# Performance work log

Measured on AMD Instinct MI355X. Metric: run time of the kernel, lower is better.

## Reference

```python
import jax, jax.numpy as jnp
import numpy as np

HEADS = 20
SHIFT = 0.6931471805599453  # style_alignment_score_shift = log(2)
KEY_SCALE = 1.0             # style_alignment_score_scale
EPS = 1e-5


def expand_first(feat, scale=1.0):
    # feat: [B, H, S, D]; broadcast style features (batch items 0 and B//2)
    b = feat.shape[0]
    fs = jnp.stack([feat[0], feat[b // 2]])[:, None]           # [2,1,H,S,D]
    fs = jnp.broadcast_to(fs, (2, b // 2) + feat.shape[1:])    # [2,B/2,H,S,D]
    if scale != 1:
        fs = jnp.concatenate([fs[:, :1], scale * fs[:, 1:]], axis=1)
    return fs.reshape(feat.shape)


def concat_first(feat, scale=1.0):
    # concatenate style features along the sequence axis (-2)
    return jnp.concatenate([feat, expand_first(feat, scale=scale)], axis=-2)


def adain(feat):
    # stats over sequence axis (-2); torch .var() is unbiased (ddof=1)
    mean = feat.mean(axis=-2, keepdims=True)
    std = jnp.sqrt(feat.var(axis=-2, keepdims=True, ddof=1) + EPS)
    sm = expand_first(mean)
    ss = expand_first(std)
    return (feat - mean) / std * ss + sm


def setup_inputs() -> dict:
    key = jax.random.key(0)
    ks = jax.random.split(key, 6)
    B, S, C = 4, 1024, 1280
    sc = 1.0 / np.sqrt(C)
    return {
        "hidden_states": jax.random.normal(ks[0], (B, S, C), jnp.float32),
        "Wq": jax.random.normal(ks[1], (C, C), jnp.float32) * sc,
        "Wk": jax.random.normal(ks[2], (C, C), jnp.float32) * sc,
        "Wv": jax.random.normal(ks[3], (C, C), jnp.float32) * sc,
        "Wo": jax.random.normal(ks[4], (C, C), jnp.float32) * sc,
        "bo": jnp.zeros((C,), jnp.float32),
    }


def reference(hidden_states, Wq, Wk, Wv, Wo, bo):
    B, S, C = hidden_states.shape
    H = HEADS
    hd = C // H
    scale = hd ** -0.5

    def to_heads(t):  # [B,S,C] -> [B,H,S,hd]
        return t.reshape(B, S, H, hd).transpose(0, 2, 1, 3)

    q = to_heads(hidden_states @ Wq.T)
    k = to_heads(hidden_states @ Wk.T)
    v = to_heads(hidden_states @ Wv.T)

    q = adain(q)              # adain_queries
    k = adain(k)              # adain_keys
    # adain_values = False

    k = concat_first(k, scale=KEY_SCALE)   # [B,H,2S,hd]
    v = concat_first(v)                    # [B,H,2S,hd]

    # shifted scaled dot-product attention (shift added to shared-key block)
    logits = jnp.einsum('bhqd,bhkd->bhqk', q, k) * scale  # [B,H,S,2S]
    bias = jnp.where(jnp.arange(k.shape[-2]) >= S, jnp.float32(SHIFT), jnp.float32(0.0))
    probs = jax.nn.softmax(logits + bias, axis=-1)
    out = jnp.einsum('bhqk,bhkd->bhqd', probs, v)         # [B,H,S,hd]

    out = out.transpose(0, 2, 1, 3).reshape(B, S, C)
    out = out @ Wo.T + bo
    return out
```

## Files before the change

kernel.cpp:

```cpp
#include <hip/hip_runtime.h>
#include <math.h>


typedef __bf16 bf16x8 __attribute__((ext_vector_type(8)));
typedef __bf16 bf16x2_t __attribute__((ext_vector_type(2)));
typedef float f32x4 __attribute__((ext_vector_type(4)));
typedef unsigned short u16x8 __attribute__((ext_vector_type(8)));

#define BDIM 256

__device__ inline unsigned short f2bf(float f) {
  return __builtin_bit_cast(unsigned short, (__bf16)f);
}
__device__ inline unsigned int pack_bf2(float lo, float hi) {
  bf16x2_t v;
  v[0] = (__bf16)lo;
  v[1] = (__bf16)hi;
  return __builtin_bit_cast(unsigned int, v);
}
__device__ inline float bf2f(unsigned short h) {
  return __uint_as_float(((unsigned int)h) << 16);
}

__device__ inline void gl_lds16(const unsigned short* g, unsigned short* l) {
  __builtin_amdgcn_global_load_lds(
      (const __attribute__((address_space(1))) unsigned int*)g,
      (__attribute__((address_space(3))) unsigned int*)l, 16, 0, 0);
}

__global__ __launch_bounds__(BDIM) void k_convert_all(
    const float* __restrict__ X, const float* __restrict__ Wq,
    const float* __restrict__ Wk, const float* __restrict__ Wv,
    const float* __restrict__ Wo, unsigned short* __restrict__ Xbf,
    unsigned short* __restrict__ Wcat, unsigned short* __restrict__ Wobf) {
  const int idx = blockIdx.x * BDIM + threadIdx.x;
  const float* src;
  unsigned short* dst;
  int off;
  if (idx < 1310720) {
    src = X; dst = Xbf; off = idx;
  } else {
    const int r = idx - 1310720;
    const int which = r / 409600;
    off = r - which * 409600;
    src = (which == 0) ? Wq : (which == 1) ? Wk : (which == 2) ? Wv : Wo;
    dst = (which < 3) ? Wcat + (size_t)which * 1638400 : Wobf;
  }
  const float4 v = ((const float4*)src)[off];
  ushort4 o;
  o.x = f2bf(v.x); o.y = f2bf(v.y); o.z = f2bf(v.z); o.w = f2bf(v.w);
  ((ushort4*)dst)[off] = o;
}

__global__ __launch_bounds__(512, 1) void k_gemm_bf16(
    const unsigned short* __restrict__ A, const unsigned short* __restrict__ B,
    unsigned short* __restrict__ Cbf, int M, int N, int K) {
  __shared__ unsigned short lds[2][2][16384];

  const int bid = blockIdx.x;
  const int swz = (bid & 7) * 30 + (bid >> 3);
  const int mt = swz & 15, nt = swz >> 4;
  const int mBase = mt * 256, nBase = nt * 256;

  const int t = threadIdx.x;
  const int w = t >> 6, lane = t & 63, quad = lane >> 4, l16 = lane & 15;
  const int wrow = w & 1, wcol = w >> 1;
  const int glg = (lane & 7) ^ ((lane >> 3) & 7);
  const int NTILES = K >> 6;

  f32x4 acc[8][4];
#pragma unroll
  for (int i = 0; i < 8; ++i)
#pragma unroll
    for (int j = 0; j < 4; ++j) acc[i][j] = (f32x4){0.f, 0.f, 0.f, 0.f};

  auto stage = [&](int s, int kt) {
#pragma unroll
    for (int j = 0; j < 4; ++j) {
      const int row = j * 64 + w * 8 + (lane >> 3);
      gl_lds16(A + (size_t)(mBase + row) * K + kt * 64 + glg * 8,
               &lds[s][0][(j * 512 + w * 64 + lane) * 8]);
    }
#pragma unroll
    for (int j = 0; j < 4; ++j) {
      const int row = j * 64 + w * 8 + (lane >> 3);
      gl_lds16(B + (size_t)(nBase + row) * K + kt * 64 + glg * 8,
               &lds[s][1][(j * 512 + w * 64 + lane) * 8]);
    }
  };

  stage(0, 0);
  stage(1, 1);
  asm volatile("s_waitcnt vmcnt(8)" ::: "memory");
  __builtin_amdgcn_s_barrier();

  const int arow0 = (wrow * 128 + l16) * 64;
  const int brow0 = (wcol * 64 + l16) * 64;
  const int g0 = ((quad) ^ (l16 & 7)) * 8;
  const int g1 = ((4 + quad) ^ (l16 & 7)) * 8;

  for (int kt = 0; kt < NTILES; ++kt) {
    const int s = kt & 1;
    if (kt >= 1 && kt + 1 < NTILES) stage(s ^ 1, kt + 1);
    const unsigned short* As = &lds[s][0][0];
    const unsigned short* Bs = &lds[s][1][0];
#pragma unroll
    for (int ph = 0; ph < 4; ++ph) {
      const int mh = ph >> 1, nh = ph & 1;
      bf16x8 af[4][2], bq[2][2];
#pragma unroll
      for (int mi = 0; mi < 4; ++mi) {
        const int ro = arow0 + (mh * 4 + mi) * 1024;
        af[mi][0] = *(const bf16x8*)(As + ro + g0);
        af[mi][1] = *(const bf16x8*)(As + ro + g1);
      }
#pragma unroll
      for (int ni = 0; ni < 2; ++ni) {
        const int ro = brow0 + (nh * 2 + ni) * 1024;
        bq[ni][0] = *(const bf16x8*)(Bs + ro + g0);
        bq[ni][1] = *(const bf16x8*)(Bs + ro + g1);
      }
      __builtin_amdgcn_s_setprio(1);
#pragma unroll
      for (int kk = 0; kk < 2; ++kk)
#pragma unroll
        for (int mi = 0; mi < 4; ++mi)
#pragma unroll
          for (int ni = 0; ni < 2; ++ni)
            acc[mh * 4 + mi][nh * 2 + ni] =
                __builtin_amdgcn_mfma_f32_16x16x32_bf16(
                    af[mi][kk], bq[ni][kk], acc[mh * 4 + mi][nh * 2 + ni], 0,
                    0, 0);
      __builtin_amdgcn_s_setprio(0);
      if (ph < 3) __builtin_amdgcn_s_barrier();
    }
    asm volatile("s_waitcnt vmcnt(0)" ::: "memory");
    __builtin_amdgcn_s_barrier();
  }

#pragma unroll
  for (int mi = 0; mi < 8; ++mi)
#pragma unroll
    for (int r = 0; r < 4; ++r) {
      const int row = mBase + wrow * 128 + mi * 16 + quad * 4 + r;
#pragma unroll
      for (int ni = 0; ni < 4; ++ni)
        Cbf[(size_t)row * N + nBase + wcol * 64 + ni * 16 + l16] =
            f2bf(acc[mi][ni][r]);
    }
}

__global__ __launch_bounds__(BDIM) void k_gemm_64x128(
    const unsigned short* __restrict__ A, const unsigned short* __restrict__ B,
    float* __restrict__ Cf, const float* __restrict__ bias, int M, int N,
    int K) {
  __shared__ unsigned short As[2][64 * 32];
  __shared__ unsigned short Bs[2][128 * 32];
  const int t = threadIdx.x;
  const int w = t >> 6, lane = t & 63, quad = lane >> 4, l16 = lane & 15;
  const int wm = (w >> 1) << 5, wn = (w & 1) << 6;
  const int mBase = blockIdx.x * 64, nBase = blockIdx.y * 128;

  f32x4 acc[2][4];
#pragma unroll
  for (int i = 0; i < 2; i++)
#pragma unroll
    for (int j = 0; j < 4; j++) acc[i][j] = (f32x4){0.f, 0.f, 0.f, 0.f};

  const int r0 = t >> 2;
  const int kk0 = (t & 3) * 8;

  for (int k0 = 0; k0 < K; k0 += 64) {
    const unsigned short* Ab = A + (size_t)(mBase + r0) * K + k0 + kk0;
    const unsigned short* Bb = B + (size_t)(nBase + r0) * K + k0 + kk0;
    gl_lds16(Ab, As[0] + t * 8);
    gl_lds16(Ab + 32, As[1] + t * 8);
    gl_lds16(Bb, Bs[0] + t * 8);
    gl_lds16(Bb + (size_t)64 * K, Bs[0] + (t + 256) * 8);
    gl_lds16(Bb + 32, Bs[1] + t * 8);
    gl_lds16(Bb + (size_t)64 * K + 32, Bs[1] + (t + 256) * 8);
    __syncthreads();
    bf16x8 af[2][2], bfr[2][4];
#pragma unroll
    for (int hh = 0; hh < 2; hh++) {
#pragma unroll
      for (int i = 0; i < 2; i++)
        af[hh][i] = *(const bf16x8*)(As[hh] + (wm + i * 16 + l16) * 32 + quad * 8);
#pragma unroll
      for (int i = 0; i < 4; i++)
        bfr[hh][i] = *(const bf16x8*)(Bs[hh] + (wn + i * 16 + l16) * 32 + quad * 8);
    }
#pragma unroll
    for (int hh = 0; hh < 2; hh++)
#pragma unroll
      for (int mi = 0; mi < 2; mi++)
#pragma unroll
        for (int ni = 0; ni < 4; ni++)
          acc[mi][ni] = __builtin_amdgcn_mfma_f32_16x16x32_bf16(
              af[hh][mi], bfr[hh][ni], acc[mi][ni], 0, 0, 0);
    __syncthreads();
  }

#pragma unroll
  for (int mi = 0; mi < 2; mi++)
#pragma unroll
    for (int r = 0; r < 4; r++) {
      const int row = mBase + wm + mi * 16 + quad * 4 + r;
#pragma unroll
      for (int ni = 0; ni < 4; ni++) {
        const int col = nBase + wn + ni * 16 + l16;
        Cf[(size_t)row * N + col] = acc[mi][ni][r] + bias[col];
      }
    }
}

__global__ __launch_bounds__(320) void k_stats1(
    const unsigned short* __restrict__ QKV, float* __restrict__ psum,
    float* __restrict__ psq) {
  const int z = blockIdx.y, which = z >> 2, b = z & 3;
  const int c = threadIdx.x * 4;
  const size_t base =
      (size_t)(b * 1024 + blockIdx.x * 32) * 3840 + which * 1280 + c;
  float4 s = {0.f, 0.f, 0.f, 0.f}, s2 = {0.f, 0.f, 0.f, 0.f};
#pragma unroll 8
  for (int i = 0; i < 32; ++i) {
    const ushort4 xv = *(const ushort4*)(QKV + base + (size_t)i * 3840);
    const float x0 = bf2f(xv.x), x1 = bf2f(xv.y), x2 = bf2f(xv.z),
                x3 = bf2f(xv.w);
    s.x += x0; s.y += x1; s.z += x2; s.w += x3;
    s2.x = fmaf(x0, x0, s2.x); s2.y = fmaf(x1, x1, s2.y);
    s2.z = fmaf(x2, x2, s2.z); s2.w = fmaf(x3, x3, s2.w);
  }
  const size_t o = ((size_t)z * 32 + blockIdx.x) * 1280 + c;
  *(float4*)(psum + o) = s;
  *(float4*)(psq + o) = s2;
}

__global__ __launch_bounds__(BDIM) void k_stats2(
    const float* __restrict__ psum, const float* __restrict__ psq,
    float* __restrict__ stats) {
  const int z = blockIdx.y, which = z >> 2, b = z & 3;
  const int c = blockIdx.x * 256 + threadIdx.x;
  float s = 0.f, s2 = 0.f;
#pragma unroll
  for (int j = 0; j < 32; ++j) {
    s += psum[((size_t)z * 32 + j) * 1280 + c];
    s2 += psq[((size_t)z * 32 + j) * 1280 + c];
  }
  const float mean = s * (1.0f / 1024.0f);
  const float var = (s2 - 1024.0f * mean * mean) * (1.0f / 1023.0f);
  stats[((which * 2 + 0) * 4 + b) * 1280 + c] = mean;
  stats[((which * 2 + 1) * 4 + b) * 1280 + c] = sqrtf(var + 1e-5f);
}

__global__ __launch_bounds__(BDIM) void k_adain_vt(
    const unsigned short* __restrict__ QKV, const float* __restrict__ stats,
    unsigned short* __restrict__ qn, unsigned short* __restrict__ kn,
    unsigned short* __restrict__ vt) {
  __shared__ unsigned short tile[64][65];
  const int bx = blockIdx.x;
  if (bx < 10240) {
    const int which = bx / 5120;
    const int rem = bx - which * 5120;
    const int b = rem / 1280;
    const int xb = rem - b * 1280;
    const int idx = xb * BDIM + threadIdx.x;
    const int s = idx / 320;
    const int c = (idx - s * 320) * 4;
    const int sb = (b < 2) ? 0 : 2;
    const ushort4 xv = *(const ushort4*)(QKV + ((size_t)(b * 1024 + s)) * 3840 +
                                         which * 1280 + c);
    const float4 mean =
        *(const float4*)(stats + ((which * 2 + 0) * 4 + b) * 1280 + c);
    const float4 stdv =
        *(const float4*)(stats + ((which * 2 + 1) * 4 + b) * 1280 + c);
    const float4 meanS =
        *(const float4*)(stats + ((which * 2 + 0) * 4 + sb) * 1280 + c);
    const float4 stdS =
        *(const float4*)(stats + ((which * 2 + 1) * 4 + sb) * 1280 + c);
    ushort4 o;
    o.x = f2bf((bf2f(xv.x) - mean.x) / stdv.x * stdS.x + meanS.x);
    o.y = f2bf((bf2f(xv.y) - mean.y) / stdv.y * stdS.y + meanS.y);
    o.z = f2bf((bf2f(xv.z) - mean.z) / stdv.z * stdS.z + meanS.z);
    o.w = f2bf((bf2f(xv.w) - mean.w) / stdv.w * stdS.w + meanS.w);
    unsigned short* dst = (which == 0) ? qn : kn;
    *(ushort4*)(dst + ((size_t)(b * 1024 + s)) * 1280 + c) = o;
  } else {
    const int tb = bx - 10240;
    const int b = tb / 320;
    const int r2 = tb - b * 320;
    const int c0 = (r2 / 16) * 64;
    const int s0 = (r2 & 15) * 64;
    const int t = threadIdx.x;
    const int r = t >> 2, seg = (t & 3) * 16;
    const size_t goff = ((size_t)(b * 1024 + s0 + r)) * 3840 + 2560 + c0 + seg;
    const u16x8 va = *(const u16x8*)(QKV + goff);
    const u16x8 vb = *(const u16x8*)(QKV + goff + 8);
#pragma unroll
    for (int j = 0; j < 8; j++) {
      tile[r][seg + j] = va[j];
      tile[r][seg + 8 + j] = vb[j];
    }
    __syncthreads();
    u16x8 o0, o1;
#pragma unroll
    for (int j = 0; j < 8; j++) {
      o0[j] = tile[seg + j][r];
      o1[j] = tile[seg + 8 + j][r];
    }
    const size_t ooff = ((size_t)(b * 1280 + c0 + r)) * 1024 + s0 + seg;
    *(u16x8*)(vt + ooff) = o0;
    *(u16x8*)(vt + ooff + 8) = o1;
  }
}

__global__ __launch_bounds__(BDIM, 4) void k_attn(
    const unsigned short* __restrict__ qn, const unsigned short* __restrict__ kn,
    const unsigned short* __restrict__ vt, unsigned short* __restrict__ Opart,
    float* __restrict__ Lpart) {
  const int S = 1024, C = 1280;
  const int L = blockIdx.x + 8 * (blockIdx.y + 20 * blockIdx.z);
  const int qt = (L >> 3) & 7;
  const int hz = (L & 7) + ((L >> 6) << 3);
  const int h = hz % 20;
  const int zs = hz / 20;
  int b, chunk;
  if (zs < 2)      { b = 0; chunk = zs; }
  else if (zs < 6) { b = 1; chunk = zs - 2; }
  else if (zs < 8) { b = 2; chunk = zs - 6; }
  else             { b = 3; chunk = zs - 8; }
  const int ktBeg = chunk * 8;
  const int t = threadIdx.x, w = t >> 6, lane = t & 63;
  const int quad = lane >> 4, l16 = lane & 15;
  const int bstyle = (b < 2) ? 0 : 2;
  const int qrow = qt * 128 + w * 32;

  __shared__ unsigned short Ks[2][2][64 * 32];
  __shared__ unsigned short Vs[2][64 * 32];
  __shared__ unsigned short Plds[4][32][64];

  bf16x8 aq[2][2];
#pragma unroll
  for (int g = 0; g < 2; ++g) {
    const size_t qoff =
        ((size_t)(b * S + qrow + g * 16 + l16)) * C + h * 64 + quad * 8;
    aq[g][0] = *(const bf16x8*)(qn + qoff);
    aq[g][1] = *(const bf16x8*)(qn + qoff + 32);
  }

  bf16x8 ones;
#pragma unroll
  for (int i = 0; i < 8; ++i) ones[i] = (__bf16)1.0f;

  f32x4 o[2][4], lsum[2];
#pragma unroll
  for (int g = 0; g < 2; ++g) {
    lsum[g] = (f32x4){0.f, 0.f, 0.f, 0.f};
#pragma unroll
    for (int i = 0; i < 4; i++) o[g][i] = (f32x4){0.f, 0.f, 0.f, 0.f};
  }

  const int krow = t >> 2;
  const int kseg = (t & 3) * 8;
  const int sw = l16 & 14;

  auto stageK = [&](int buf, int kt) {
    const int bs = (kt < 16) ? b : bstyle;
    const int sk = (kt & 15) * 64;
    const unsigned short* kg =
        kn + (size_t)(bs * S + sk + krow) * C + h * 64 + kseg;
    gl_lds16(kg, Ks[buf][0] + t * 8);
    gl_lds16(kg + 32, Ks[buf][1] + t * 8);
  };
  auto stageV = [&](int kt) {
    const int bs = (kt < 16) ? b : bstyle;
    const int sk = (kt & 15) * 64;
    const unsigned short* vg =
        vt + (size_t)(bs * C + h * 64 + krow) * S + sk + kseg;
    gl_lds16(vg, Vs[0] + t * 8);
    gl_lds16(vg + 32, Vs[1] + t * 8);
  };

  stageK(0, ktBeg);

  const float SCALE2 = 0.125f * 1.44269504088896341f;

  for (int i = 0; i < 8; ++i) {
    const int kt = ktBeg + i;
    const int buf = i & 1;
    __syncthreads();
    stageV(kt);
    if (i + 1 < 8) stageK(buf ^ 1, kt + 1);

    const float bias2 = (kt >= 16) ? 1.0f : 0.0f;

    f32x4 z2[2][4];
#pragma unroll
    for (int nt = 0; nt < 4; ++nt) {
      const bf16x8 bk0 =
          *(const bf16x8*)(Ks[buf][0] + (nt * 16 + l16) * 32 + quad * 8);
      const bf16x8 bk1 =
          *(const bf16x8*)(Ks[buf][1] + (nt * 16 + l16) * 32 + quad * 8);
#pragma unroll
      for (int g = 0; g < 2; ++g) {
        f32x4 zz = (f32x4){0.f, 0.f, 0.f, 0.f};
        zz = __builtin_amdgcn_mfma_f32_16x16x32_bf16(bk0, aq[g][0], zz, 0, 0, 0);
        zz = __builtin_amdgcn_mfma_f32_16x16x32_bf16(bk1, aq[g][1], zz, 0, 0, 0);
        z2[g][nt] = zz;
      }
    }

#pragma unroll
    for (int g = 0; g < 2; ++g) {
#pragma unroll
      for (int nt = 0; nt < 4; ++nt) {
        const float e0 = exp2f(fmaf(z2[g][nt][0], SCALE2, bias2));
        const float e1 = exp2f(fmaf(z2[g][nt][1], SCALE2, bias2));
        const float e2 = exp2f(fmaf(z2[g][nt][2], SCALE2, bias2));
        const float e3 = exp2f(fmaf(z2[g][nt][3], SCALE2, bias2));
        uint2 pk;
        pk.x = pack_bf2(e0, e1);
        pk.y = pack_bf2(e2, e3);
        const int phys = (nt * 4 + quad) ^ sw;
        *(uint2*)(&Plds[w][g * 16 + l16][phys * 4]) = pk;
      }
    }

    __syncthreads();

#pragma unroll
    for (int g = 0; g < 2; ++g) {
      const int a0 = (2 * quad) ^ sw;
      const int a1 = (2 * quad + 8) ^ sw;
      const bf16x8 pa0 = *(const bf16x8*)(&Plds[w][g * 16 + l16][a0 * 4]);
      const bf16x8 pa1 = *(const bf16x8*)(&Plds[w][g * 16 + l16][a1 * 4]);
      lsum[g] = __builtin_amdgcn_mfma_f32_16x16x32_bf16(pa0, ones, lsum[g], 0, 0, 0);
      lsum[g] = __builtin_amdgcn_mfma_f32_16x16x32_bf16(pa1, ones, lsum[g], 0, 0, 0);
#pragma unroll
      for (int dt = 0; dt < 4; ++dt) {
        const bf16x8 vb0 =
            *(const bf16x8*)(Vs[0] + (dt * 16 + l16) * 32 + quad * 8);
        const bf16x8 vb1 =
            *(const bf16x8*)(Vs[1] + (dt * 16 + l16) * 32 + quad * 8);
        o[g][dt] =
            __builtin_amdgcn_mfma_f32_16x16x32_bf16(pa0, vb0, o[g][dt], 0, 0, 0);
        o[g][dt] =
            __builtin_amdgcn_mfma_f32_16x16x32_bf16(pa1, vb1, o[g][dt], 0, 0, 0);
      }
    }
  }

  if (l16 == 0) {
#pragma unroll
    for (int g = 0; g < 2; ++g)
#pragma unroll
      for (int r = 0; r < 4; ++r)
        Lpart[((size_t)zs * 20 + h) * 1024 + qrow + g * 16 + quad * 4 + r] =
            lsum[g][r];
  }

  unsigned short* Op = Opart + (size_t)zs * 1024 * 1280;
#pragma unroll
  for (int g = 0; g < 2; ++g)
#pragma unroll
    for (int dt = 0; dt < 4; ++dt)
#pragma unroll
      for (int r = 0; r < 4; ++r)
        Op[(size_t)(qrow + g * 16 + quad * 4 + r) * 1280 + h * 64 + dt * 16 +
           l16] = f2bf(o[g][dt][r]);
}

__global__ __launch_bounds__(BDIM) void k_combine(
    const unsigned short* __restrict__ Opart, const float* __restrict__ Lpart,
    unsigned short* __restrict__ attnb) {
  const int idx = blockIdx.x * BDIM + threadIdx.x;
  const int row = idx / 160;
  const int c = (idx - row * 160) * 8;
  const int b = row >> 10, q = row & 1023, h = c >> 6;
  const int zb = (b >> 1) * 6 + (b & 1) * 2;
  const int ns = 2 + (b & 1) * 2;
  float L = 0.f;
  float acc[8] = {0.f, 0.f, 0.f, 0.f, 0.f, 0.f, 0.f, 0.f};
  for (int s = 0; s < ns; ++s) {
    L += Lpart[((size_t)(zb + s) * 20 + h) * 1024 + q];
    const u16x8 v =
        *(const u16x8*)(Opart + (size_t)(zb + s) * 1310720 + (size_t)q * 1280 + c);
#pragma unroll
    for (int j = 0; j < 8; ++j) acc[j] += bf2f(v[j]);
  }
  const float rl = 1.0f / L;
  u16x8 o8;
#pragma unroll
  for (int j = 0; j < 8; ++j) o8[j] = f2bf(acc[j] * rl);
  *(u16x8*)(attnb + (size_t)row * 1280 + c) = o8;
}

extern "C" void kernel_launch(void* const* d_in, const int* in_sizes, int n_in,
                              void* d_out, int out_size, void* d_ws,
                              size_t ws_size, hipStream_t stream) {
  const float* X = (const float*)d_in[0];
  const float* Wq = (const float*)d_in[1];
  const float* Wk = (const float*)d_in[2];
  const float* Wv = (const float*)d_in[3];
  const float* Wo = (const float*)d_in[4];
  const float* bo = (const float*)d_in[5];
  float* out = (float*)d_out;

  char* ws = (char*)d_ws;
  size_t off = 0;
  auto alloc = [&](size_t bytes) {
    char* p = ws + off;
    off += (bytes + 255) & ~(size_t)255;
    return p;
  };
  unsigned short* Wcat = (unsigned short*)alloc(3840ull * 1280 * 2);
  unsigned short* Xbf = (unsigned short*)alloc(4096ull * 1280 * 2);
  unsigned short* QKV = (unsigned short*)alloc(4096ull * 3840 * 2);
  unsigned short* Wobf = (unsigned short*)alloc(1280ull * 1280 * 2);
  float* stats = (float*)alloc(2ull * 2 * 4 * 1280 * 4);
  unsigned short* qnb = (unsigned short*)alloc(4096ull * 1280 * 2);
  unsigned short* knb = (unsigned short*)alloc(4096ull * 1280 * 2);
  unsigned short* vtb = (unsigned short*)alloc(4096ull * 1280 * 2);
  unsigned short* attnb = (unsigned short*)alloc(4096ull * 1280 * 2);

  unsigned short* Opart = QKV;
  float* Lpart = (float*)Wcat;
  float* psum = (float*)attnb;
  float* psq = (float*)(attnb + 4096ull * 1280 / 2);

  k_convert_all<<<11520, BDIM, 0, stream>>>(X, Wq, Wk, Wv, Wo, Xbf, Wcat, Wobf);
  k_gemm_bf16<<<240, 512, 0, stream>>>(Xbf, Wcat, QKV, 4096, 3840, 1280);
  k_stats1<<<dim3(32, 8), 320, 0, stream>>>(QKV, psum, psq);
  k_stats2<<<dim3(5, 8), BDIM, 0, stream>>>(psum, psq, stats);
  k_adain_vt<<<11520, BDIM, 0, stream>>>(QKV, stats, qnb, knb, vtb);
  k_attn<<<dim3(8, 20, 12), BDIM, 0, stream>>>(qnb, knb, vtb, Opart, Lpart);
  k_combine<<<2560, BDIM, 0, stream>>>(Opart, Lpart, attnb);
  k_gemm_64x128<<<dim3(64, 10), BDIM, 0, stream>>>(attnb, Wobf, out, bo, 4096,
                                                   1280, 1280);
}
```

Before: 263.4 us.

## Retile output GEMM to 128x128 with prefetch pipeline and shrink attention P buffer

Replaces the 64x128 output projection GEMM with a 128x128 tile kernel. The new kernel double-buffers K tiles, prefetching the next tile while computing the current one. It also uses XOR-swizzled LDS addressing, a block-index swizzle for cache locality, and MFMA priority hints. This is meant to raise operand reuse and overlap loads with MFMA work. The attention kernel now writes and consumes the probability tile one 16-row group at a time, halving its per-warp LDS buffer so it can target five blocks per CU. The risks are that 320 large tiles may fill the GPU unevenly, and that the serialized P handling adds latency inside each wave.

```diff
diff --git a/kernel.cpp b/kernel.cpp
--- a/kernel.cpp
+++ b/kernel.cpp
@@ -150,65 +150,98 @@
     }
 }
 
-__global__ __launch_bounds__(BDIM) void k_gemm_64x128(
+__global__ __launch_bounds__(BDIM, 2) void k_gemm_out(
     const unsigned short* __restrict__ A, const unsigned short* __restrict__ B,
     float* __restrict__ Cf, const float* __restrict__ bias, int M, int N,
     int K) {
-  __shared__ unsigned short As[2][64 * 32];
-  __shared__ unsigned short Bs[2][128 * 32];
+  __shared__ unsigned short lds[2][2][8192];
+
+  const int bid = blockIdx.x;
+  const int swz = (bid & 7) * 40 + (bid >> 3);
+  const int mt = swz & 31, nt = swz >> 5;
+  const int mBase = mt * 128, nBase = nt * 128;
+
   const int t = threadIdx.x;
   const int w = t >> 6, lane = t & 63, quad = lane >> 4, l16 = lane & 15;
-  const int wm = (w >> 1) << 5, wn = (w & 1) << 6;
-  const int mBase = blockIdx.x * 64, nBase = blockIdx.y * 128;
-
-  f32x4 acc[2][4];
-#pragma unroll
-  for (int i = 0; i < 2; i++)
-#pragma unroll
-    for (int j = 0; j < 4; j++) acc[i][j] = (f32x4){0.f, 0.f, 0.f, 0.f};
-
-  const int r0 = t >> 2;
-  const int kk0 = (t & 3) * 8;
-
-  for (int k0 = 0; k0 < K; k0 += 64) {
-    const unsigned short* Ab = A + (size_t)(mBase + r0) * K + k0 + kk0;
-    const unsigned short* Bb = B + (size_t)(nBase + r0) * K + k0 + kk0;
-    gl_lds16(Ab, As[0] + t * 8);
-    gl_lds16(Ab + 32, As[1] + t * 8);
-    gl_lds16(Bb, Bs[0] + t * 8);
-    gl_lds16(Bb + (size_t)64 * K, Bs[0] + (t + 256) * 8);
-    gl_lds16(Bb + 32, Bs[1] + t * 8);
-    gl_lds16(Bb + (size_t)64 * K + 32, Bs[1] + (t + 256) * 8);
-    __syncthreads();
-    bf16x8 af[2][2], bfr[2][4];
-#pragma unroll
-    for (int hh = 0; hh < 2; hh++) {
-#pragma unroll
-      for (int i = 0; i < 2; i++)
-        af[hh][i] = *(const bf16x8*)(As[hh] + (wm + i * 16 + l16) * 32 + quad * 8);
-#pragma unroll
-      for (int i = 0; i < 4; i++)
-        bfr[hh][i] = *(const bf16x8*)(Bs[hh] + (wn + i * 16 + l16) * 32 + quad * 8);
-    }
-#pragma unroll
-    for (int hh = 0; hh < 2; hh++)
-#pragma unroll
-      for (int mi = 0; mi < 2; mi++)
-#pragma unroll
-        for (int ni = 0; ni < 4; ni++)
-          acc[mi][ni] = __builtin_amdgcn_mfma_f32_16x16x32_bf16(
-              af[hh][mi], bfr[hh][ni], acc[mi][ni], 0, 0, 0);
-    __syncthreads();
-  }
-
-#pragma unroll
-  for (int mi = 0; mi < 2; mi++)
-#pragma unroll
-    for (int r = 0; r < 4; r++) {
-      const int row = mBase + wm + mi * 16 + quad * 4 + r;
-#pragma unroll
-      for (int ni = 0; ni < 4; ni++) {
-        const int col = nBase + wn + ni * 16 + l16;
+  const int wrow = w & 1, wcol = w >> 1;
+  const int glg = (lane & 7) ^ ((lane >> 3) & 7);
+  const int NTILES = K >> 6;
+
+  f32x4 acc[4][4];
+#pragma unroll
+  for (int i = 0; i < 4; ++i)
+#pragma unroll
+    for (int j = 0; j < 4; ++j) acc[i][j] = (f32x4){0.f, 0.f, 0.f, 0.f};
+
+  auto stage = [&](int s, int kt) {
+#pragma unroll
+    for (int j = 0; j < 4; ++j) {
+      const int row = j * 32 + (t >> 3);
+      gl_lds16(A + (size_t)(mBase + row) * K + kt * 64 + glg * 8,
+               &lds[s][0][(j * 256 + t) * 8]);
+    }
+#pragma unroll
+    for (int j = 0; j < 4; ++j) {
+      const int row = j * 32 + (t >> 3);
+      gl_lds16(B + (size_t)(nBase + row) * K + kt * 64 + glg * 8,
+               &lds[s][1][(j * 256 + t) * 8]);
+    }
+  };
+
+  stage(0, 0);
+  stage(1, 1);
+  asm volatile("s_waitcnt vmcnt(8)" ::: "memory");
+  __builtin_amdgcn_s_barrier();
+
+  const int arow0 = (wrow * 64 + l16) * 64;
+  const int brow0 = (wcol * 64 + l16) * 64;
+  const int g0 = ((quad) ^ (l16 & 7)) * 8;
+  const int g1 = ((4 + quad) ^ (l16 & 7)) * 8;
+
+  for (int kt = 0; kt < NTILES; ++kt) {
+    const int s = kt & 1;
+    if (kt >= 1 && kt + 1 < NTILES) stage(s ^ 1, kt + 1);
+    const unsigned short* As = &lds[s][0][0];
+    const unsigned short* Bs = &lds[s][1][0];
+#pragma unroll
+    for (int ph = 0; ph < 2; ++ph) {
+      bf16x8 af[2][2], bq[4][2];
+#pragma unroll
+      for (int mi = 0; mi < 2; ++mi) {
+        const int ro = arow0 + (ph * 2 + mi) * 1024;
+        af[mi][0] = *(const bf16x8*)(As + ro + g0);
+        af[mi][1] = *(const bf16x8*)(As + ro + g1);
+      }
+#pragma unroll
+      for (int ni = 0; ni < 4; ++ni) {
+        const int ro = brow0 + ni * 1024;
+        bq[ni][0] = *(const bf16x8*)(Bs + ro + g0);
+        bq[ni][1] = *(const bf16x8*)(Bs + ro + g1);
+      }
+      __builtin_amdgcn_s_setprio(1);
+#pragma unroll
+      for (int kk = 0; kk < 2; ++kk)
+#pragma unroll
+        for (int mi = 0; mi < 2; ++mi)
+#pragma unroll
+          for (int ni = 0; ni < 4; ++ni)
+            acc[ph * 2 + mi][ni] = __builtin_amdgcn_mfma_f32_16x16x32_bf16(
+                af[mi][kk], bq[ni][kk], acc[ph * 2 + mi][ni], 0, 0, 0);
+      __builtin_amdgcn_s_setprio(0);
+      if (ph == 0) __builtin_amdgcn_s_barrier();
+    }
+    asm volatile("s_waitcnt vmcnt(0)" ::: "memory");
+    __builtin_amdgcn_s_barrier();
+  }
+
+#pragma unroll
+  for (int mi = 0; mi < 4; ++mi)
+#pragma unroll
+    for (int r = 0; r < 4; ++r) {
+      const int row = mBase + wrow * 64 + mi * 16 + quad * 4 + r;
+#pragma unroll
+      for (int ni = 0; ni < 4; ++ni) {
+        const int col = nBase + wcol * 64 + ni * 16 + l16;
         Cf[(size_t)row * N + col] = acc[mi][ni][r] + bias[col];
       }
     }
@@ -314,7 +347,7 @@
   }
 }
 
-__global__ __launch_bounds__(BDIM, 4) void k_attn(
+__global__ __launch_bounds__(BDIM, 5) void k_attn(
     const unsigned short* __restrict__ qn, const unsigned short* __restrict__ kn,
     const unsigned short* __restrict__ vt, unsigned short* __restrict__ Opart,
     float* __restrict__ Lpart) {
@@ -337,7 +370,7 @@
 
   __shared__ unsigned short Ks[2][2][64 * 32];
   __shared__ unsigned short Vs[2][64 * 32];
-  __shared__ unsigned short Plds[4][32][64];
+  __shared__ unsigned short Plds[4][16][64];
 
   bf16x8 aq[2][2];
 #pragma unroll
@@ -410,8 +443,7 @@
       }
     }
 
-#pragma unroll
-    for (int g = 0; g < 2; ++g) {
+    auto packwrite = [&](int g) {
 #pragma unroll
       for (int nt = 0; nt < 4; ++nt) {
         const float e0 = exp2f(fmaf(z2[g][nt][0], SCALE2, bias2));
@@ -422,20 +454,18 @@
         pk.x = pack_bf2(e0, e1);
         pk.y = pack_bf2(e2, e3);
         const int phys = (nt * 4 + quad) ^ sw;
-        *(uint2*)(&Plds[w][g * 16 + l16][phys * 4]) = pk;
-      }
-    }
-
-    __syncthreads();
-
-#pragma unroll
-    for (int g = 0; g < 2; ++g) {
+        *(uint2*)(&Plds[w][l16][phys * 4]) = pk;
+      }
+    };
+    auto pv = [&](int g) {
       const int a0 = (2 * quad) ^ sw;
       const int a1 = (2 * quad + 8) ^ sw;
-      const bf16x8 pa0 = *(const bf16x8*)(&Plds[w][g * 16 + l16][a0 * 4]);
-      const bf16x8 pa1 = *(const bf16x8*)(&Plds[w][g * 16 + l16][a1 * 4]);
-      lsum[g] = __builtin_amdgcn_mfma_f32_16x16x32_bf16(pa0, ones, lsum[g], 0, 0, 0);
-      lsum[g] = __builtin_amdgcn_mfma_f32_16x16x32_bf16(pa1, ones, lsum[g], 0, 0, 0);
+      const bf16x8 pa0 = *(const bf16x8*)(&Plds[w][l16][a0 * 4]);
+      const bf16x8 pa1 = *(const bf16x8*)(&Plds[w][l16][a1 * 4]);
+      lsum[g] =
+          __builtin_amdgcn_mfma_f32_16x16x32_bf16(pa0, ones, lsum[g], 0, 0, 0);
+      lsum[g] =
+          __builtin_amdgcn_mfma_f32_16x16x32_bf16(pa1, ones, lsum[g], 0, 0, 0);
 #pragma unroll
       for (int dt = 0; dt < 4; ++dt) {
         const bf16x8 vb0 =
@@ -447,7 +477,13 @@
         o[g][dt] =
             __builtin_amdgcn_mfma_f32_16x16x32_bf16(pa1, vb1, o[g][dt], 0, 0, 0);
       }
-    }
+    };
+
+    packwrite(0);
+    __syncthreads();
+    pv(0);
+    packwrite(1);
+    pv(1);
   }
 
   if (l16 == 0) {
@@ -535,6 +571,5 @@
   k_adain_vt<<<11520, BDIM, 0, stream>>>(QKV, stats, qnb, knb, vtb);
   k_attn<<<dim3(8, 20, 12), BDIM, 0, stream>>>(qnb, knb, vtb, Opart, Lpart);
   k_combine<<<2560, BDIM, 0, stream>>>(Opart, Lpart, attnb);
-  k_gemm_64x128<<<dim3(64, 10), BDIM, 0, stream>>>(attnb, Wobf, out, bo, 4096,
-                                                   1280, 1280);
-}
+  k_gemm_out<<<320, BDIM, 0, stream>>>(attnb, Wobf, out, bo, 4096, 1280, 1280);
+}
```

Result: slower. 325.4 us (+23.5%).
